# Kernel tuning notes

Hardware: AMD Instinct MI355X
Metric: run time of the kernel (lower is better)

Reference implementation:

```python
import jax, jax.numpy as jnp
import numpy as np

NUM_HEADS = 4
OUTPUT_DIM = 32
NUM_NODES = 50000
NUM_EDGES = 800000
INPUT_DIM = 128


def setup_inputs() -> dict:
    key = jax.random.key(0)
    k1, k2, k3, k4 = jax.random.split(key, 4)
    node_features = jax.random.uniform(k1, (NUM_NODES, INPUT_DIM), dtype=jnp.float32)
    edge_index = jax.random.randint(k2, (2, NUM_EDGES), 0, NUM_NODES, dtype=jnp.int64)
    # Linear weight (xavier-like scale), stored as [in, out] for x @ W
    W = jax.random.normal(k3, (INPUT_DIM, NUM_HEADS * OUTPUT_DIM), dtype=jnp.float32) * 0.1
    att = jax.random.normal(k4, (2 * OUTPUT_DIM, 1), dtype=jnp.float32) * 0.2
    return {"node_features": node_features, "edge_index": edge_index, "W": W, "att": att}


def reference(node_features, edge_index, W, att):
    num_nodes = node_features.shape[0]
    # Linear projection -> [N, H, D]  (dropout = identity in eval mode)
    proj = (node_features @ W).reshape(num_nodes, NUM_HEADS, OUTPUT_DIM)
    src = proj[edge_index[0]]   # [E, H, D]
    tgt = proj[edge_index[1]]   # [E, H, D]
    # concat([src,tgt]) @ att  ==  src @ att[:D] + tgt @ att[D:]
    a_src = att[:OUTPUT_DIM, 0]   # [D]
    a_tgt = att[OUTPUT_DIM:, 0]   # [D]
    scores = jax.nn.leaky_relu(
        jnp.einsum('ehd,d->eh', src, a_src) + jnp.einsum('ehd,d->eh', tgt, a_tgt),
        negative_slope=0.01,
    )  # [E, H]
    # Faithful to original: softmax over the HEADS axis (dim=-1 of [E, H])
    alpha = jax.nn.softmax(scores, axis=-1)  # [E, H]
    weighted = tgt * alpha[..., None]        # [E, H, D]
    # index_add_ on dim 0 with edge_index[0]
    out = jax.ops.segment_sum(weighted, edge_index[0], num_segments=num_nodes)  # [N, H, D]
    # concat_heads=False -> mean over heads
    return out.mean(axis=1)  # [N, D]
```

## Files before the change

kernel.cpp:

```cpp
#include <hip/hip_runtime.h>
#include <math.h>

#define N_NODES 50000
#define N_EDGES 800000
#define IN_DIM 128
#define N_HEADS 4
#define OUT_DIM 32
#define PROJ_DIM 128
#define WSTR 144

#define NBIN 782
#define BINCAP 1408
#define MAXDEG 64

#define PROJ_BLKS 391
#define PART_BLKS 391
#define FUSE_BLKS (NBIN + PROJ_BLKS)

typedef short bf16x8 __attribute__((ext_vector_type(8)));
typedef float f32x4  __attribute__((ext_vector_type(4)));
typedef _Float16 h2  __attribute__((ext_vector_type(2)));

__device__ __forceinline__ ushort f32_to_bf16(float f) {
    unsigned u = __float_as_uint(f);
    unsigned r = u + 0x7fffu + ((u >> 16) & 1u);
    return (ushort)(r >> 16);
}

__device__ __forceinline__ bf16x8 cvt8(float4 a, float4 b) {
    bf16x8 r;
    r[0] = (short)f32_to_bf16(a.x); r[1] = (short)f32_to_bf16(a.y);
    r[2] = (short)f32_to_bf16(a.z); r[3] = (short)f32_to_bf16(a.w);
    r[4] = (short)f32_to_bf16(b.x); r[5] = (short)f32_to_bf16(b.y);
    r[6] = (short)f32_to_bf16(b.z); r[7] = (short)f32_to_bf16(b.w);
    return r;
}

__device__ __forceinline__ ushort f32_to_f16(float f) {
    return __builtin_bit_cast(ushort, (_Float16)f);
}

__global__ __launch_bounds__(256) void partition_kernel(
    const int* __restrict__ ei, int* __restrict__ bin_cursor,
    unsigned* __restrict__ slab)
{
    __shared__ int cnt[NBIN];
    __shared__ int gbase[NBIN];

    const int tid = threadIdx.x;

    for (int t = tid; t < NBIN; t += 256) cnt[t] = 0;
    __syncthreads();

    const int ebase = blockIdx.x * 2048;
    unsigned srcv[8], tgtv[8];
    int rank[8];
#pragma unroll
    for (int i = 0; i < 8; ++i) {
        int e = ebase + i * 256 + tid;
        bool ok = e < N_EDGES;
        srcv[i] = ok ? (unsigned)ei[e] : 0u;
        tgtv[i] = ok ? (unsigned)ei[N_EDGES + e] : 0u;
        rank[i] = ok ? atomicAdd(&cnt[srcv[i] >> 6], 1) : -1;
    }
    __syncthreads();

    for (int t = tid; t < NBIN; t += 256)
        gbase[t] = atomicAdd(&bin_cursor[t], cnt[t]);
    __syncthreads();

#pragma unroll
    for (int i = 0; i < 8; ++i) {
        if (rank[i] >= 0) {
            int bin = srcv[i] >> 6;
            int p = gbase[bin] + rank[i];
            if (p < BINCAP)
                slab[bin * BINCAP + p] = (tgtv[i] << 16) | (srcv[i] & 63u);
        }
    }
}

__global__ __launch_bounds__(256) void fused_kernel(
    const float* __restrict__ X, const float* __restrict__ W,
    const float* __restrict__ att,
    const unsigned* __restrict__ slab, const int* __restrict__ bin_cursor,
    ushort* __restrict__ projT, float* __restrict__ s_src, float* __restrict__ s_tgt,
    ushort* __restrict__ csr, int* __restrict__ offs, int* __restrict__ deg)
{
    __shared__ ushort Wt[128 * WSTR];

    const int tid = threadIdx.x;

    if (blockIdx.x < NBIN) {
        int*    cnt2 = (int*)Wt;
        int*    ex   = cnt2 + 64;
        ushort* stgt = (ushort*)(ex + 64);

        const int b = blockIdx.x;
        const int t = tid;
        int n_e = bin_cursor[b];
        n_e = (n_e < BINCAP) ? n_e : BINCAP;

        if (t < 64) cnt2[t] = 0;
        __syncthreads();

        unsigned pk[6];
        int npk = 0;
        for (int i = t; i < n_e; i += 256) {
            unsigned v = slab[b * BINCAP + i];
            int node6 = v & 63u;
            int r = atomicAdd(&cnt2[node6], 1);
            r = (r < 255) ? r : 255;
            pk[npk++] = (v & 0xFFFF0000u) | ((unsigned)r << 8) | (unsigned)node6;
        }
        __syncthreads();

        if (t < 64) {
            int v = cnt2[t];
            int x = v;
#pragma unroll
            for (int off = 1; off < 64; off <<= 1) {
                int y = __shfl_up(x, off);
                x += (t >= off) ? y : 0;
            }
            ex[t] = x - v;
        }
        __syncthreads();

        for (int j = 0; j < npk; ++j) {
            unsigned pv = pk[j];
            int lpos = ex[pv & 63u] + (int)((pv >> 8) & 255u);
            if (lpos < BINCAP) stgt[lpos] = (ushort)(pv >> 16);
        }
        __syncthreads();

        for (int i = t; i < n_e; i += 256) csr[b * BINCAP + i] = stgt[i];
        int node = b * 64 + t;
        if (t < 64 && node < N_NODES) {
            offs[node] = b * BINCAP + ex[t];
            deg[node]  = cnt2[t];
        }
        return;
    }

    for (int idx = tid; idx < 64 * 128; idx += 256) {
        int kp = idx >> 7;
        int c  = idx & 127;
        float w0 = W[(2 * kp) * PROJ_DIM + c];
        float w1 = W[(2 * kp + 1) * PROJ_DIM + c];
        unsigned pr = (unsigned)f32_to_bf16(w0) | ((unsigned)f32_to_bf16(w1) << 16);
        *(unsigned*)&Wt[c * WSTR + 2 * kp] = pr;
    }
    __syncthreads();

    const int wv   = tid >> 6;
    const int lane = tid & 63;
    const int m = lane & 15;
    const int q = lane >> 4;
    const int rbase = (blockIdx.x - NBIN) * 128;

    int arow0 = rbase + wv * 32 + m;
    int arow1 = arow0 + 16;
    arow0 = (arow0 < N_NODES) ? arow0 : N_NODES - 1;
    arow1 = (arow1 < N_NODES) ? arow1 : N_NODES - 1;
    const long long xb0 = (long long)arow0 * IN_DIM;
    const long long xb1 = (long long)arow1 * IN_DIM;

    f32x4 acc[2][8];
#pragma unroll
    for (int rt = 0; rt < 2; ++rt)
#pragma unroll
        for (int ct = 0; ct < 8; ++ct) acc[rt][ct] = (f32x4){0.f, 0.f, 0.f, 0.f};

#pragma unroll
    for (int ks = 0; ks < 4; ++ks) {
        const int k0 = ks * 32 + q * 8;
        float4 a0lo = *(const float4*)&X[xb0 + k0];
        float4 a0hi = *(const float4*)&X[xb0 + k0 + 4];
        float4 a1lo = *(const float4*)&X[xb1 + k0];
        float4 a1hi = *(const float4*)&X[xb1 + k0 + 4];
        bf16x8 afrag0 = cvt8(a0lo, a0hi);
        bf16x8 afrag1 = cvt8(a1lo, a1hi);
#pragma unroll
        for (int ct = 0; ct < 8; ++ct) {
            bf16x8 bfrag = *(const bf16x8*)&Wt[(ct * 16 + m) * WSTR + k0];
            acc[0][ct] = __builtin_amdgcn_mfma_f32_16x16x32_bf16(afrag0, bfrag, acc[0][ct], 0, 0, 0);
            acc[1][ct] = __builtin_amdgcn_mfma_f32_16x16x32_bf16(afrag1, bfrag, acc[1][ct], 0, 0, 0);
        }
    }

    const float as_lo = att[m],      as_hi = att[m + 16];
    const float at_lo = att[32 + m], at_hi = att[48 + m];

#pragma unroll
    for (int rt = 0; rt < 2; ++rt) {
        const int rowb = rbase + wv * 32 + rt * 16 + q * 4;
#pragma unroll
        for (int r = 0; r < 4; ++r) {
            const int row = rowb + r;
            float cl[4], ch[4];
#pragma unroll
            for (int h = 0; h < 4; ++h) {
                cl[h] = acc[rt][2 * h][r];
                ch[h] = acc[rt][2 * h + 1][r];
            }
            if (row < N_NODES) {
                ushort4 plo, phi;
                plo.x = f32_to_f16(cl[0]); plo.y = f32_to_f16(cl[1]);
                plo.z = f32_to_f16(cl[2]); plo.w = f32_to_f16(cl[3]);
                phi.x = f32_to_f16(ch[0]); phi.y = f32_to_f16(ch[1]);
                phi.z = f32_to_f16(ch[2]); phi.w = f32_to_f16(ch[3]);
                *(ushort4*)&projT[(long long)row * PROJ_DIM + m * 4] = plo;
                *(ushort4*)&projT[(long long)row * PROJ_DIM + (m + 16) * 4] = phi;
            }
            float ps[4], pt[4];
#pragma unroll
            for (int h = 0; h < 4; ++h) {
                ps[h] = cl[h] * as_lo + ch[h] * as_hi;
                pt[h] = cl[h] * at_lo + ch[h] * at_hi;
            }
#pragma unroll
            for (int off = 8; off > 0; off >>= 1) {
#pragma unroll
                for (int h = 0; h < 4; ++h) {
                    ps[h] += __shfl_down(ps[h], off, 16);
                    pt[h] += __shfl_down(pt[h], off, 16);
                }
            }
            if (m == 0 && row < N_NODES) {
                *(float4*)&s_src[row * N_HEADS] = make_float4(ps[0], ps[1], ps[2], ps[3]);
                *(float4*)&s_tgt[row * N_HEADS] = make_float4(pt[0], pt[1], pt[2], pt[3]);
            }
        }
    }
}

__global__ __launch_bounds__(256) void gather_kernel(
    const int* __restrict__ deg, const int* __restrict__ offs,
    const ushort* __restrict__ csr,
    const float* __restrict__ s_src, const float* __restrict__ s_tgt,
    const ushort* __restrict__ projT, float* __restrict__ out)
{
    __shared__ uint4 edata[4][MAXDEG];

    const int wv   = threadIdx.x >> 6;
    const int lane = threadIdx.x & 63;
    const int node = blockIdx.x * 4 + wv;

    int n = deg[node];
    n = (n < MAXDEG) ? n : MAXDEG;
    const int o = offs[node];

    uint4 ed = make_uint4(0u, 0u, 0u, 0u);
    if (lane < n) {
        int tgt = csr[o + lane];
        float4 ss = *(const float4*)&s_src[node * N_HEADS];
        float4 st = *(const float4*)&s_tgt[tgt * N_HEADS];

        float sc[4] = { ss.x + st.x, ss.y + st.y, ss.z + st.z, ss.w + st.w };
        float mx = -1e30f;
#pragma unroll
        for (int h = 0; h < 4; ++h) {
            sc[h] = (sc[h] > 0.0f) ? sc[h] : 0.01f * sc[h];
            mx = fmaxf(mx, sc[h]);
        }
        float sum = 0.0f;
#pragma unroll
        for (int h = 0; h < 4; ++h) {
            sc[h] = __expf(sc[h] - mx);
            sum += sc[h];
        }
        float inv = 0.25f / sum;

        h2 a01, a23;
        a01.x = (_Float16)(sc[0] * inv);
        a01.y = (_Float16)(sc[1] * inv);
        a23.x = (_Float16)(sc[2] * inv);
        a23.y = (_Float16)(sc[3] * inv);
        ed.x = (unsigned)tgt;
        ed.y = __builtin_bit_cast(unsigned, a01);
        ed.z = __builtin_bit_cast(unsigned, a23);
    }
    edata[wv][lane] = ed;

    const int d    = lane & 31;
    const int half = lane >> 5;

    float acc0 = 0.0f, acc1 = 0.0f, acc2 = 0.0f, acc3 = 0.0f;

    for (int j = 0; j < n; j += 16) {
        uint4 s[8];
#pragma unroll
        for (int u = 0; u < 8; ++u)
            s[u] = edata[wv][j + 2 * u + half];
        uint2 p[8];
#pragma unroll
        for (int u = 0; u < 8; ++u)
            p[u] = *(const uint2*)&projT[(long long)s[u].x * PROJ_DIM + d * 4];
#pragma unroll
        for (int u = 0; u < 8; ++u) {
            h2 a  = __builtin_bit_cast(h2, s[u].y);
            h2 b  = __builtin_bit_cast(h2, s[u].z);
            h2 lo = __builtin_bit_cast(h2, p[u].x);
            h2 hi = __builtin_bit_cast(h2, p[u].y);
            float* accp = (u & 1) ? ((u & 2) ? &acc3 : &acc1)
                                  : ((u & 2) ? &acc2 : &acc0);
            float tt = *accp;
#if __has_builtin(__builtin_amdgcn_fdot2)
            tt = __builtin_amdgcn_fdot2(a, lo, tt, false);
            tt = __builtin_amdgcn_fdot2(b, hi, tt, false);
#else
            tt = fmaf((float)a.x, (float)lo.x, tt);
            tt = fmaf((float)a.y, (float)lo.y, tt);
            tt = fmaf((float)b.x, (float)hi.x, tt);
            tt = fmaf((float)b.y, (float)hi.y, tt);
#endif
            *accp = tt;
        }
    }

    float acc = (acc0 + acc1) + (acc2 + acc3);
    acc += __shfl_down(acc, 32);
    if (lane < 32) out[node * OUT_DIM + d] = acc;
}

extern "C" void kernel_launch(void* const* d_in, const int* in_sizes, int n_in,
                              void* d_out, int out_size, void* d_ws, size_t ws_size,
                              hipStream_t stream) {
    const float* X   = (const float*)d_in[0];
    const int*   ei  = (const int*)d_in[1];
    const float* W   = (const float*)d_in[2];
    const float* att = (const float*)d_in[3];
    float* out = (float*)d_out;

    char* p = (char*)d_ws;
    ushort* projT   = (ushort*)p;   p += (size_t)N_NODES * PROJ_DIM * 2;
    float* s_src    = (float*)p;    p += (size_t)N_NODES * N_HEADS * 4;
    float* s_tgt    = (float*)p;    p += (size_t)N_NODES * N_HEADS * 4;
    unsigned* slab  = (unsigned*)p; p += (size_t)NBIN * BINCAP * 4;
    ushort* csr     = (ushort*)p;   p += (size_t)NBIN * BINCAP * 2;
    int* offs       = (int*)p;      p += (size_t)N_NODES * 4;
    int* deg        = (int*)p;      p += (size_t)N_NODES * 4;
    int* bin_cursor = (int*)p;      p += 1024 * 4;

    (void)hipMemsetAsync(bin_cursor, 0, NBIN * sizeof(int), stream);

    partition_kernel<<<PART_BLKS, 256, 0, stream>>>(ei, bin_cursor, slab);

    fused_kernel<<<FUSE_BLKS, 256, 0, stream>>>(
        X, W, att, slab, bin_cursor, projT, s_src, s_tgt, csr, offs, deg);

    gather_kernel<<<N_NODES / 4, 256, 0, stream>>>(
        deg, offs, csr, s_src, s_tgt, projT, out);
}
```

Before: 148.7 us.

## Coarsen partition bins to 256 nodes, split CSR build into quarter blocks

The partition kernel now buckets edges by source into 196 bins of 256 nodes instead of 782 bins of 64. This cuts shared-memory counters and the global atomics on bin cursors per partition block. The CSR-building stage launches four blocks per bin, and each block scans the whole bin slab but keeps only edges for its 64-node quarter. The trade-off is that every bin slab is read four times, and the per-thread register array grows to 20 entries.

After: 149.1 us. Within noise of the previous version (+0.2%).

```diff
diff --git a/kernel.cpp b/kernel.cpp
--- a/kernel.cpp
+++ b/kernel.cpp
@@ -9,13 +9,15 @@
 #define PROJ_DIM 128
 #define WSTR 144
 
-#define NBIN 782
-#define BINCAP 1408
+#define NBIN 196
+#define BINCAP 5000
+#define NQBLK (NBIN * 4)
+#define QCAP 1408
 #define MAXDEG 64
 
 #define PROJ_BLKS 391
 #define PART_BLKS 391
-#define FUSE_BLKS (NBIN + PROJ_BLKS)
+#define FUSE_BLKS (NQBLK + PROJ_BLKS)
 
 typedef short bf16x8 __attribute__((ext_vector_type(8)));
 typedef float f32x4  __attribute__((ext_vector_type(4)));
@@ -44,8 +46,8 @@
     const int* __restrict__ ei, int* __restrict__ bin_cursor,
     unsigned* __restrict__ slab)
 {
-    __shared__ int cnt[NBIN];
-    __shared__ int gbase[NBIN];
+    __shared__ int cnt[256];
+    __shared__ int gbase[256];
 
     const int tid = threadIdx.x;
 
@@ -61,7 +63,7 @@
         bool ok = e < N_EDGES;
         srcv[i] = ok ? (unsigned)ei[e] : 0u;
         tgtv[i] = ok ? (unsigned)ei[N_EDGES + e] : 0u;
-        rank[i] = ok ? atomicAdd(&cnt[srcv[i] >> 6], 1) : -1;
+        rank[i] = ok ? atomicAdd(&cnt[srcv[i] >> 8], 1) : -1;
     }
     __syncthreads();
 
@@ -72,10 +74,10 @@
 #pragma unroll
     for (int i = 0; i < 8; ++i) {
         if (rank[i] >= 0) {
-            int bin = srcv[i] >> 6;
+            int bin = srcv[i] >> 8;
             int p = gbase[bin] + rank[i];
             if (p < BINCAP)
-                slab[bin * BINCAP + p] = (tgtv[i] << 16) | (srcv[i] & 63u);
+                slab[bin * BINCAP + p] = (tgtv[i] << 16) | (srcv[i] & 255u);
         }
     }
 }
@@ -91,27 +93,33 @@
 
     const int tid = threadIdx.x;
 
-    if (blockIdx.x < NBIN) {
+    if (blockIdx.x < NQBLK) {
         int*    cnt2 = (int*)Wt;
         int*    ex   = cnt2 + 64;
-        ushort* stgt = (ushort*)(ex + 64);
-
-        const int b = blockIdx.x;
-        const int t = tid;
-        int n_e = bin_cursor[b];
+        int*    tot  = ex + 64;
+        ushort* stgt = (ushort*)(tot + 4);
+
+        const int b   = blockIdx.x;
+        const int bin = b >> 2;
+        const int qtr = b & 3;
+        const int t   = tid;
+        int n_e = bin_cursor[bin];
         n_e = (n_e < BINCAP) ? n_e : BINCAP;
 
         if (t < 64) cnt2[t] = 0;
         __syncthreads();
 
-        unsigned pk[6];
+        unsigned pk[20];
         int npk = 0;
         for (int i = t; i < n_e; i += 256) {
-            unsigned v = slab[b * BINCAP + i];
-            int node6 = v & 63u;
-            int r = atomicAdd(&cnt2[node6], 1);
-            r = (r < 255) ? r : 255;
-            pk[npk++] = (v & 0xFFFF0000u) | ((unsigned)r << 8) | (unsigned)node6;
+            unsigned v = slab[bin * BINCAP + i];
+            int node8 = v & 255u;
+            if ((node8 >> 6) == qtr) {
+                int idx = node8 & 63;
+                int r = atomicAdd(&cnt2[idx], 1);
+                r = (r < 255) ? r : 255;
+                pk[npk++] = (v & 0xFFFF0000u) | ((unsigned)r << 8) | (unsigned)idx;
+            }
         }
         __syncthreads();
 
@@ -124,20 +132,23 @@
                 x += (t >= off) ? y : 0;
             }
             ex[t] = x - v;
+            if (t == 63) *tot = x;
         }
         __syncthreads();
 
         for (int j = 0; j < npk; ++j) {
             unsigned pv = pk[j];
             int lpos = ex[pv & 63u] + (int)((pv >> 8) & 255u);
-            if (lpos < BINCAP) stgt[lpos] = (ushort)(pv >> 16);
+            if (lpos < QCAP) stgt[lpos] = (ushort)(pv >> 16);
         }
         __syncthreads();
 
-        for (int i = t; i < n_e; i += 256) csr[b * BINCAP + i] = stgt[i];
-        int node = b * 64 + t;
+        int qn = *tot;
+        qn = (qn < QCAP) ? qn : QCAP;
+        for (int i = t; i < qn; i += 256) csr[b * QCAP + i] = stgt[i];
+        int node = bin * 256 + qtr * 64 + t;
         if (t < 64 && node < N_NODES) {
-            offs[node] = b * BINCAP + ex[t];
+            offs[node] = b * QCAP + ex[t];
             deg[node]  = cnt2[t];
         }
         return;
@@ -157,7 +168,7 @@
     const int lane = tid & 63;
     const int m = lane & 15;
     const int q = lane >> 4;
-    const int rbase = (blockIdx.x - NBIN) * 128;
+    const int rbase = (blockIdx.x - NQBLK) * 128;
 
     int arow0 = rbase + wv * 32 + m;
     int arow1 = arow0 + 16;
@@ -338,12 +349,12 @@
     float* s_src    = (float*)p;    p += (size_t)N_NODES * N_HEADS * 4;
     float* s_tgt    = (float*)p;    p += (size_t)N_NODES * N_HEADS * 4;
     unsigned* slab  = (unsigned*)p; p += (size_t)NBIN * BINCAP * 4;
-    ushort* csr     = (ushort*)p;   p += (size_t)NBIN * BINCAP * 2;
+    ushort* csr     = (ushort*)p;   p += (size_t)NQBLK * QCAP * 2;
     int* offs       = (int*)p;      p += (size_t)N_NODES * 4;
     int* deg        = (int*)p;      p += (size_t)N_NODES * 4;
-    int* bin_cursor = (int*)p;      p += 1024 * 4;
-
-    (void)hipMemsetAsync(bin_cursor, 0, NBIN * sizeof(int), stream);
+    int* bin_cursor = (int*)p;      p += 256 * 4;
+
+    (void)hipMemsetAsync(bin_cursor, 0, 256 * sizeof(int), stream);
 
     partition_kernel<<<PART_BLKS, 256, 0, stream>>>(ei, bin_cursor, slab);
 
```
